# Performance work log

Measured on AMD Instinct MI355X. Metric: run time of the kernel, lower is better.

Reference implementation:

```python
import jax, jax.numpy as jnp
import numpy as np

B, IN, OUT = 8192, 4096, 4096
EPS = 1e-4


def setup_inputs() -> dict:
    key = jax.random.key(0)
    k1, k2 = jax.random.split(key)
    x = jax.random.normal(k1, (B, IN), dtype=jnp.float32)
    gamma = jnp.ones((IN,), dtype=jnp.float32)
    beta = jnp.zeros((IN,), dtype=jnp.float32)
    weight = jax.random.normal(k2, (OUT, IN), dtype=jnp.float32) * 0.02
    bias = jnp.zeros((OUT,), dtype=jnp.float32)
    return {"x": x, "gamma": gamma, "beta": beta, "weight": weight, "bias": bias}


def bin_weight(w):
    # center per output row, clamp, L1-scale, sign (2D branch of BinWeightFn)
    wc = jnp.clip(w - jnp.mean(w, axis=1, keepdims=True), -1.0, 1.0)
    n = w.shape[1]
    scale = jnp.sum(jnp.abs(wc), axis=1, keepdims=True) / n  # [out, 1]
    return jnp.sign(wc), scale


def reference(x, gamma, beta, weight, bias):
    # BatchNorm1d in training mode: batch statistics (biased variance)
    mu = jnp.mean(x, axis=0)
    var = jnp.var(x, axis=0)
    xn = (x - mu) / jnp.sqrt(var + EPS) * gamma + beta
    # binarize activations and weights
    x_bin = jnp.sign(xn)
    w_bin, scale = bin_weight(weight)
    # binary GEMM + bias, then per-output-channel L1 scale, then ReLU
    y = x_bin @ w_bin.T + bias          # [B, OUT]
    y = y * scale.reshape(1, -1)
    return jax.nn.relu(y)
```

## Files before the change

kernel.cpp:

```cpp
#include <hip/hip_runtime.h>
#include <stdint.h>

#define BATCH 8192
#define IN 4096
#define OUT 4096
#define EPS 1e-4f
#define RCHUNK 128
#define NCHUNKS (BATCH / RCHUNK)

typedef int v4i __attribute__((ext_vector_type(4)));

#define AS1(p) ((const __attribute__((address_space(1))) void*)(p))
#define AS3(p) ((__attribute__((address_space(3))) void*)(p))

__global__ __launch_bounds__(256) void colstat_partial(
    const float* __restrict__ x, float* __restrict__ P1, float* __restrict__ P2) {
    int col = blockIdx.x * 256 + threadIdx.x;
    int r0 = blockIdx.y * RCHUNK;
    float s1 = 0.f, s2 = 0.f;
    const float* p = x + (size_t)r0 * IN + col;
    for (int r = 0; r < RCHUNK; ++r) {
        float v = p[(size_t)r * IN];
        s1 += v;
        s2 += v * v;
    }
    P1[blockIdx.y * IN + col] = s1;
    P2[blockIdx.y * IN + col] = s2;
}

__global__ __launch_bounds__(256) void colstat_final(
    const float* __restrict__ P1, const float* __restrict__ P2,
    const float* __restrict__ gamma, float* __restrict__ mu, float* __restrict__ aArr) {
    int col = blockIdx.x * 256 + threadIdx.x;
    double s1 = 0.0, s2 = 0.0;
    for (int c = 0; c < NCHUNKS; ++c) {
        s1 += (double)P1[c * IN + col];
        s2 += (double)P2[c * IN + col];
    }
    double m = s1 / (double)BATCH;
    double var = s2 / (double)BATCH - m * m;
    float rstd = (float)(1.0 / sqrt(var + (double)EPS));
    mu[col] = (float)m;
    aArr[col] = rstd * gamma[col];
}

__global__ __launch_bounds__(256) void binx8(
    const float* __restrict__ x, const float* __restrict__ mu,
    const float* __restrict__ aArr, const float* __restrict__ beta,
    uint8_t* __restrict__ x01, int* __restrict__ px) {
    __shared__ int red[4];
    int r = blockIdx.x;
    int tid = threadIdx.x;
    int lane = tid & 63;
    int wv = tid >> 6;
    const float4* row = (const float4*)(x + (size_t)r * IN);
    const float4* m4 = (const float4*)mu;
    const float4* a4 = (const float4*)aArr;
    const float4* b4 = (const float4*)beta;
    uchar4* o4 = (uchar4*)(x01 + (size_t)r * IN);
    int cnt = 0;
#pragma unroll
    for (int it = 0; it < IN / 1024; ++it) {
        int q = it * 256 + tid;
        float4 v = row[q];
        float4 m = m4[q];
        float4 a = a4[q];
        float4 b = b4[q];
        uchar4 ob;
        ob.x = (uint8_t)((v.x - m.x) * a.x + b.x > 0.f);
        ob.y = (uint8_t)((v.y - m.y) * a.y + b.y > 0.f);
        ob.z = (uint8_t)((v.z - m.z) * a.z + b.z > 0.f);
        ob.w = (uint8_t)((v.w - m.w) * a.w + b.w > 0.f);
        cnt += (int)ob.x + (int)ob.y + (int)ob.z + (int)ob.w;
        o4[q] = ob;
    }
    for (int off = 32; off > 0; off >>= 1) cnt += __shfl_down(cnt, off, 64);
    if (lane == 0) red[wv] = cnt;
    __syncthreads();
    if (tid == 0) px[r] = red[0] + red[1] + red[2] + red[3];
}

__global__ __launch_bounds__(256) void binw8(
    const float* __restrict__ w, uint8_t* __restrict__ w01,
    float* __restrict__ scale, int* __restrict__ pw) {
    __shared__ double redd[4];
    __shared__ int redi[4];
    __shared__ double bcast;
    int o = blockIdx.x;
    int tid = threadIdx.x;
    int lane = tid & 63;
    int wv = tid >> 6;
    const float4* row = (const float4*)(w + (size_t)o * IN);
    uchar4* o4 = (uchar4*)(w01 + (size_t)o * IN);

    float4 vs[4];
    float part = 0.f;
#pragma unroll
    for (int it = 0; it < 4; ++it) {
        vs[it] = row[it * 256 + tid];
        part += vs[it].x + vs[it].y + vs[it].z + vs[it].w;
    }
    double d = (double)part;
    for (int off = 32; off > 0; off >>= 1) d += __shfl_down(d, off, 64);
    if (lane == 0) redd[wv] = d;
    __syncthreads();
    if (tid == 0) bcast = (redd[0] + redd[1] + redd[2] + redd[3]) / (double)IN;
    __syncthreads();
    float mean = (float)bcast;

    float absacc = 0.f;
    int cnt = 0;
#pragma unroll
    for (int it = 0; it < 4; ++it) {
        float4 v = vs[it];
        float wcx = v.x - mean, wcy = v.y - mean, wcz = v.z - mean, wcw = v.w - mean;
        uchar4 ob;
        ob.x = (uint8_t)(wcx > 0.f);
        ob.y = (uint8_t)(wcy > 0.f);
        ob.z = (uint8_t)(wcz > 0.f);
        ob.w = (uint8_t)(wcw > 0.f);
        cnt += (int)ob.x + (int)ob.y + (int)ob.z + (int)ob.w;
        absacc += fminf(fabsf(wcx), 1.0f) + fminf(fabsf(wcy), 1.0f) +
                  fminf(fabsf(wcz), 1.0f) + fminf(fabsf(wcw), 1.0f);
        o4[it * 256 + tid] = ob;
    }
    double da = (double)absacc;
    for (int off = 32; off > 0; off >>= 1) da += __shfl_down(da, off, 64);
    for (int off = 32; off > 0; off >>= 1) cnt += __shfl_down(cnt, off, 64);
    if (lane == 0) { redd[wv] = da; redi[wv] = cnt; }
    __syncthreads();
    if (tid == 0) {
        scale[o] = (float)((redd[0] + redd[1] + redd[2] + redd[3]) / (double)IN);
        pw[o] = redi[0] + redi[1] + redi[2] + redi[3];
    }
}

#define BM 128
#define BN 128
#define BKI 64
__global__ __launch_bounds__(256, 2) void bgemm_i8(
    const uint8_t* __restrict__ x01, const uint8_t* __restrict__ w01,
    const int* __restrict__ px, const int* __restrict__ pw,
    const float* __restrict__ scale, const float* __restrict__ bias,
    float* __restrict__ out) {
    __shared__ uint8_t As[BM * BKI];
    __shared__ uint8_t Bs[BN * BKI];

    int tid = threadIdx.x;
    int lane = tid & 63;
    int wave = tid >> 6;
    int rowBlk = blockIdx.y * BM;
    int colBlk = blockIdx.x * BN;
    int wm = (wave >> 1) * 64;
    int wn = (wave & 1) * 64;

    v4i acc[4][4];
#pragma unroll
    for (int i = 0; i < 4; ++i)
#pragma unroll
        for (int j = 0; j < 4; ++j) acc[i][j] = (v4i){0, 0, 0, 0};

    const uint8_t* ag = x01 + (size_t)rowBlk * IN;
    const uint8_t* bg = w01 + (size_t)colBlk * IN;

    int lrow = lane & 15;
    int lk = (lane >> 4) * 16;

    for (int kc = 0; kc < IN / BKI; ++kc) {
#pragma unroll
        for (int it = 0; it < 2; ++it) {
            int idx = tid + it * 256;
            int r = idx >> 2;
            int ch = idx & 3;
            __builtin_amdgcn_global_load_lds(
                AS1(ag + (size_t)r * IN + kc * BKI + ch * 16),
                AS3(As + idx * 16), 16, 0, 0);
            __builtin_amdgcn_global_load_lds(
                AS1(bg + (size_t)r * IN + kc * BKI + ch * 16),
                AS3(Bs + idx * 16), 16, 0, 0);
        }
        __syncthreads();

        v4i af[4], bf[4];
#pragma unroll
        for (int i = 0; i < 4; ++i)
            af[i] = *(const v4i*)(As + (wm + i * 16 + lrow) * BKI + lk);
#pragma unroll
        for (int j = 0; j < 4; ++j)
            bf[j] = *(const v4i*)(Bs + (wn + j * 16 + lrow) * BKI + lk);
#pragma unroll
        for (int i = 0; i < 4; ++i)
#pragma unroll
            for (int j = 0; j < 4; ++j)
                acc[i][j] = __builtin_amdgcn_mfma_i32_16x16x64_i8(af[i], bf[j], acc[i][j], 0, 0, 0);
        __syncthreads();
    }

    int crow0 = (lane >> 4) * 4;
    int ccol = lane & 15;
#pragma unroll
    for (int i = 0; i < 4; ++i) {
        int rbase = rowBlk + wm + i * 16 + crow0;
        int pxr[4];
#pragma unroll
        for (int rg = 0; rg < 4; ++rg) pxr[rg] = px[rbase + rg];
#pragma unroll
        for (int j = 0; j < 4; ++j) {
            int cb = colBlk + wn + j * 16 + ccol;
            float sc = scale[cb];
            float bs = bias[cb];
            int pwc = pw[cb];
#pragma unroll
            for (int rg = 0; rg < 4; ++rg) {
                int dot = 4 * acc[i][j][rg] - 2 * pxr[rg] - 2 * pwc + IN;
                float y = ((float)dot + bs) * sc;
                out[(size_t)(rbase + rg) * OUT + cb] = y > 0.f ? y : 0.f;
            }
        }
    }
}

extern "C" void kernel_launch(void* const* d_in, const int* in_sizes, int n_in,
                              void* d_out, int out_size, void* d_ws, size_t ws_size,
                              hipStream_t stream) {
    const float* x = (const float*)d_in[0];
    const float* gamma = (const float*)d_in[1];
    const float* beta = (const float*)d_in[2];
    const float* weight = (const float*)d_in[3];
    const float* bias = (const float*)d_in[4];
    float* out = (float*)d_out;

    char* w = (char*)d_ws;
    float* mu = (float*)(w);
    float* aArr = (float*)(w + 16384);
    float* scale = (float*)(w + 32768);
    int* px = (int*)(w + 49152);
    int* pw = (int*)(w + 81920);
    float* P1 = (float*)(w + (1 << 20));
    float* P2 = (float*)(w + (2 << 20));
    uint8_t* x01 = (uint8_t*)(w + (4 << 20));
    uint8_t* w01 = (uint8_t*)(w + (36 << 20));

    colstat_partial<<<dim3(IN / 256, NCHUNKS), 256, 0, stream>>>(x, P1, P2);
    colstat_final<<<dim3(IN / 256), 256, 0, stream>>>(P1, P2, gamma, mu, aArr);
    binx8<<<dim3(BATCH), 256, 0, stream>>>(x, mu, aArr, beta, x01, px);
    binw8<<<dim3(OUT), 256, 0, stream>>>(weight, w01, scale, pw);
    bgemm_i8<<<dim3(OUT / BN, BATCH / BM), 256, 0, stream>>>(x01, w01, px, pw, scale, bias, out);
}
```

Baseline: 450.3 us.

## Rewrite int8 binary GEMM as 256x256 tile ping-pong pipelined kernel

Replaces the 128x128 single-buffered int8 MFMA GEMM with a 512-thread 256x256 tile kernel. It uses double-buffered 128KB LDS with XOR-swizzled layout, interleaved async global-to-LDS staging, manual barriers and vmcnt waits, setprio around MFMA bursts, and a swizzled block order for L2 reuse. It also vectorizes the column-stat partial kernel to float4. The aim is to hide load latency, cut LDS bank conflicts and raise arithmetic intensity. The cost is heavy register use, one block per CU of LDS, and fragile hand-tuned wait counts.

After: 412.2 us. 8.4% less time.

```diff
diff --git a/kernel.cpp b/kernel.cpp
--- a/kernel.cpp
+++ b/kernel.cpp
@@ -9,23 +9,24 @@
 #define NCHUNKS (BATCH / RCHUNK)
 
 typedef int v4i __attribute__((ext_vector_type(4)));
+typedef unsigned char u8;
 
 #define AS1(p) ((const __attribute__((address_space(1))) void*)(p))
 #define AS3(p) ((__attribute__((address_space(3))) void*)(p))
 
 __global__ __launch_bounds__(256) void colstat_partial(
     const float* __restrict__ x, float* __restrict__ P1, float* __restrict__ P2) {
-    int col = blockIdx.x * 256 + threadIdx.x;
+    int c4 = blockIdx.x * 256 + threadIdx.x;
     int r0 = blockIdx.y * RCHUNK;
-    float s1 = 0.f, s2 = 0.f;
-    const float* p = x + (size_t)r0 * IN + col;
+    float4 s1 = {0.f, 0.f, 0.f, 0.f}, s2 = {0.f, 0.f, 0.f, 0.f};
+    const float4* p = (const float4*)x + (size_t)r0 * (IN / 4) + c4;
     for (int r = 0; r < RCHUNK; ++r) {
-        float v = p[(size_t)r * IN];
-        s1 += v;
-        s2 += v * v;
-    }
-    P1[blockIdx.y * IN + col] = s1;
-    P2[blockIdx.y * IN + col] = s2;
+        float4 v = p[(size_t)r * (IN / 4)];
+        s1.x += v.x; s1.y += v.y; s1.z += v.z; s1.w += v.w;
+        s2.x += v.x * v.x; s2.y += v.y * v.y; s2.z += v.z * v.z; s2.w += v.w * v.w;
+    }
+    ((float4*)P1)[blockIdx.y * (IN / 4) + c4] = s1;
+    ((float4*)P2)[blockIdx.y * (IN / 4) + c4] = s2;
 }
 
 __global__ __launch_bounds__(256) void colstat_final(
@@ -47,7 +48,7 @@
 __global__ __launch_bounds__(256) void binx8(
     const float* __restrict__ x, const float* __restrict__ mu,
     const float* __restrict__ aArr, const float* __restrict__ beta,
-    uint8_t* __restrict__ x01, int* __restrict__ px) {
+    u8* __restrict__ x01, int* __restrict__ px) {
     __shared__ int red[4];
     int r = blockIdx.x;
     int tid = threadIdx.x;
@@ -67,10 +68,10 @@
         float4 a = a4[q];
         float4 b = b4[q];
         uchar4 ob;
-        ob.x = (uint8_t)((v.x - m.x) * a.x + b.x > 0.f);
-        ob.y = (uint8_t)((v.y - m.y) * a.y + b.y > 0.f);
-        ob.z = (uint8_t)((v.z - m.z) * a.z + b.z > 0.f);
-        ob.w = (uint8_t)((v.w - m.w) * a.w + b.w > 0.f);
+        ob.x = (u8)((v.x - m.x) * a.x + b.x > 0.f);
+        ob.y = (u8)((v.y - m.y) * a.y + b.y > 0.f);
+        ob.z = (u8)((v.z - m.z) * a.z + b.z > 0.f);
+        ob.w = (u8)((v.w - m.w) * a.w + b.w > 0.f);
         cnt += (int)ob.x + (int)ob.y + (int)ob.z + (int)ob.w;
         o4[q] = ob;
     }
@@ -81,7 +82,7 @@
 }
 
 __global__ __launch_bounds__(256) void binw8(
-    const float* __restrict__ w, uint8_t* __restrict__ w01,
+    const float* __restrict__ w, u8* __restrict__ w01,
     float* __restrict__ scale, int* __restrict__ pw) {
     __shared__ double redd[4];
     __shared__ int redi[4];
@@ -115,10 +116,10 @@
         float4 v = vs[it];
         float wcx = v.x - mean, wcy = v.y - mean, wcz = v.z - mean, wcw = v.w - mean;
         uchar4 ob;
-        ob.x = (uint8_t)(wcx > 0.f);
-        ob.y = (uint8_t)(wcy > 0.f);
-        ob.z = (uint8_t)(wcz > 0.f);
-        ob.w = (uint8_t)(wcw > 0.f);
+        ob.x = (u8)(wcx > 0.f);
+        ob.y = (u8)(wcy > 0.f);
+        ob.z = (u8)(wcz > 0.f);
+        ob.w = (u8)(wcw > 0.f);
         cnt += (int)ob.x + (int)ob.y + (int)ob.z + (int)ob.w;
         absacc += fminf(fabsf(wcx), 1.0f) + fminf(fabsf(wcy), 1.0f) +
                   fminf(fabsf(wcz), 1.0f) + fminf(fabsf(wcw), 1.0f);
@@ -135,78 +136,146 @@
     }
 }
 
-#define BM 128
-#define BN 128
-#define BKI 64
-__global__ __launch_bounds__(256, 2) void bgemm_i8(
-    const uint8_t* __restrict__ x01, const uint8_t* __restrict__ w01,
+#define BKB 128
+#define NKT (IN / BKB)
+#define NIT (NKT / 2)
+
+#define STG_A(t, q, p) __builtin_amdgcn_global_load_lds( \
+    AS1(ag + (size_t)((q)*64 + slr) * IN + (t)*BKB + sswz), \
+    AS3(lds + (p)*65536 + (q)*8192 + sdst), 16, 0, 0)
+#define STG_B(t, q, p) __builtin_amdgcn_global_load_lds( \
+    AS1(bg + (size_t)((q)*64 + slr) * IN + (t)*BKB + sswz), \
+    AS3(lds + (p)*65536 + 32768 + (q)*8192 + sdst), 16, 0, 0)
+
+#define LOADA(p, rh) do { \
+    _Pragma("unroll") for (int i_ = 0; i_ < 4; ++i_) \
+    _Pragma("unroll") for (int k_ = 0; k_ < 2; ++k_) \
+        af[i_][k_] = *(const v4i*)(lds + (p)*65536 + aBase + (rh)*8192 + i_*2048 + swk[k_]); \
+} while (0)
+#define LOADB(p, ch) do { \
+    _Pragma("unroll") for (int j_ = 0; j_ < 2; ++j_) \
+    _Pragma("unroll") for (int k_ = 0; k_ < 2; ++k_) \
+        bf[j_][k_] = *(const v4i*)(lds + (p)*65536 + bBase + (ch)*4096 + j_*2048 + swk[k_]); \
+} while (0)
+#define MMA(rh, ch) do { \
+    __builtin_amdgcn_s_setprio(1); \
+    _Pragma("unroll") for (int i_ = 0; i_ < 4; ++i_) \
+    _Pragma("unroll") for (int j_ = 0; j_ < 2; ++j_) \
+    _Pragma("unroll") for (int k_ = 0; k_ < 2; ++k_) \
+        acc[(rh)*4 + i_][(ch)*2 + j_] = __builtin_amdgcn_mfma_i32_16x16x64_i8( \
+            af[i_][k_], bf[j_][k_], acc[(rh)*4 + i_][(ch)*2 + j_], 0, 0, 0); \
+    __builtin_amdgcn_s_setprio(0); \
+} while (0)
+#define BAR() asm volatile("s_barrier" ::: "memory")
+#define VM(n) asm volatile("s_waitcnt vmcnt(" #n ")" ::: "memory")
+
+__global__ __launch_bounds__(512, 2) void bgemm_i8(
+    const u8* __restrict__ x01, const u8* __restrict__ w01,
     const int* __restrict__ px, const int* __restrict__ pw,
     const float* __restrict__ scale, const float* __restrict__ bias,
     float* __restrict__ out) {
-    __shared__ uint8_t As[BM * BKI];
-    __shared__ uint8_t Bs[BN * BKI];
+    __shared__ u8 lds[131072];
 
     int tid = threadIdx.x;
     int lane = tid & 63;
     int wave = tid >> 6;
-    int rowBlk = blockIdx.y * BM;
-    int colBlk = blockIdx.x * BN;
-    int wm = (wave >> 1) * 64;
-    int wn = (wave & 1) * 64;
-
-    v4i acc[4][4];
-#pragma unroll
-    for (int i = 0; i < 4; ++i)
+    int wm = wave >> 2;
+    int wn = wave & 3;
+
+    int lin = blockIdx.y * (OUT / 256) + blockIdx.x;
+    int swz = (lin & 7) * 64 + (lin >> 3);
+    int colBlk = (swz & 15) * 256;
+    int rowBlk = (swz >> 4) * 256;
+
+    const u8* ag = x01 + (size_t)rowBlk * IN;
+    const u8* bg = w01 + (size_t)colBlk * IN;
+
+    int slr = tid >> 3;
+    int ss = tid & 7;
+    int sswz = (ss ^ (slr & 7)) * 16;
+    int sdst = slr * 128 + ss * 16;
+
+    int lrow = lane & 15;
+    int lhi = lane >> 4;
+    int llo = lane & 7;
+    int swk[2] = { ((lhi) ^ llo) * 16, ((4 + lhi) ^ llo) * 16 };
+    int aBase = (wm * 128 + lrow) * 128;
+    int bBase = 32768 + (wn * 64 + lrow) * 128;
+
+    v4i acc[8][4];
+#pragma unroll
+    for (int i = 0; i < 8; ++i)
 #pragma unroll
         for (int j = 0; j < 4; ++j) acc[i][j] = (v4i){0, 0, 0, 0};
-
-    const uint8_t* ag = x01 + (size_t)rowBlk * IN;
-    const uint8_t* bg = w01 + (size_t)colBlk * IN;
-
-    int lrow = lane & 15;
-    int lk = (lane >> 4) * 16;
-
-    for (int kc = 0; kc < IN / BKI; ++kc) {
-#pragma unroll
-        for (int it = 0; it < 2; ++it) {
-            int idx = tid + it * 256;
-            int r = idx >> 2;
-            int ch = idx & 3;
-            __builtin_amdgcn_global_load_lds(
-                AS1(ag + (size_t)r * IN + kc * BKI + ch * 16),
-                AS3(As + idx * 16), 16, 0, 0);
-            __builtin_amdgcn_global_load_lds(
-                AS1(bg + (size_t)r * IN + kc * BKI + ch * 16),
-                AS3(Bs + idx * 16), 16, 0, 0);
-        }
-        __syncthreads();
-
-        v4i af[4], bf[4];
-#pragma unroll
-        for (int i = 0; i < 4; ++i)
-            af[i] = *(const v4i*)(As + (wm + i * 16 + lrow) * BKI + lk);
-#pragma unroll
-        for (int j = 0; j < 4; ++j)
-            bf[j] = *(const v4i*)(Bs + (wn + j * 16 + lrow) * BKI + lk);
-#pragma unroll
-        for (int i = 0; i < 4; ++i)
-#pragma unroll
-            for (int j = 0; j < 4; ++j)
-                acc[i][j] = __builtin_amdgcn_mfma_i32_16x16x64_i8(af[i], bf[j], acc[i][j], 0, 0, 0);
-        __syncthreads();
-    }
-
-    int crow0 = (lane >> 4) * 4;
-    int ccol = lane & 15;
-#pragma unroll
-    for (int i = 0; i < 4; ++i) {
-        int rbase = rowBlk + wm + i * 16 + crow0;
+    v4i af[4][2], bf[2][2];
+
+    STG_A(0, 0, 0); STG_A(0, 1, 0); STG_A(0, 2, 0); STG_A(0, 3, 0);
+    STG_B(0, 0, 0); STG_B(0, 1, 0); STG_B(0, 2, 0); STG_B(0, 3, 0);
+    STG_A(1, 0, 1); STG_A(1, 2, 1);
+    VM(2);
+    BAR();
+
+    for (int j = 0; j < NIT - 1; ++j) {
+        int O = 2 * j + 1, E2 = 2 * j + 2, O2 = 2 * j + 3;
+        LOADA(0, 0); LOADB(0, 0);
+        STG_B(O, 0, 1); STG_B(O, 1, 1);
+        BAR(); MMA(0, 0); BAR();
+        LOADB(0, 1);
+        STG_B(O, 2, 1); STG_B(O, 3, 1);
+        BAR(); MMA(0, 1); VM(6); BAR();
+        LOADA(0, 1); LOADB(0, 0);
+        STG_A(O, 1, 1); STG_A(O, 3, 1); STG_A(E2, 0, 0); STG_A(E2, 2, 0);
+        BAR(); MMA(1, 0); BAR();
+        LOADB(0, 1);
+        BAR(); MMA(1, 1); VM(4); BAR();
+        LOADA(1, 0); LOADB(1, 0);
+        STG_B(E2, 0, 0); STG_B(E2, 1, 0);
+        BAR(); MMA(0, 0); BAR();
+        LOADB(1, 1);
+        STG_B(E2, 2, 0); STG_B(E2, 3, 0);
+        BAR(); MMA(0, 1); VM(4); BAR();
+        LOADA(1, 1); LOADB(1, 0);
+        STG_A(E2, 1, 0); STG_A(E2, 3, 0);
+        BAR(); MMA(1, 0); BAR();
+        LOADB(1, 1);
+        STG_A(O2, 0, 1); STG_A(O2, 2, 1);
+        BAR(); MMA(1, 1); VM(4); BAR();
+    }
+
+    {
+        int O = NKT - 1;
+        LOADA(0, 0); LOADB(0, 0);
+        STG_B(O, 0, 1); STG_B(O, 1, 1);
+        BAR(); MMA(0, 0); BAR();
+        LOADB(0, 1);
+        STG_B(O, 2, 1); STG_B(O, 3, 1);
+        BAR(); MMA(0, 1); VM(6); BAR();
+        LOADA(0, 1); LOADB(0, 0);
+        STG_A(O, 1, 1); STG_A(O, 3, 1);
+        BAR(); MMA(1, 0); BAR();
+        LOADB(0, 1);
+        BAR(); MMA(1, 1); VM(2); BAR();
+        LOADA(1, 0); LOADB(1, 0);
+        BAR(); MMA(0, 0); BAR();
+        LOADB(1, 1);
+        BAR(); MMA(0, 1); VM(0); BAR();
+        LOADA(1, 1); LOADB(1, 0);
+        BAR(); MMA(1, 0); BAR();
+        LOADB(1, 1);
+        BAR(); MMA(1, 1); BAR();
+    }
+
+    int crow0 = lhi * 4;
+    int ccol = lrow;
+#pragma unroll
+    for (int i = 0; i < 8; ++i) {
+        int rbase = rowBlk + wm * 128 + i * 16 + crow0;
         int pxr[4];
 #pragma unroll
         for (int rg = 0; rg < 4; ++rg) pxr[rg] = px[rbase + rg];
 #pragma unroll
         for (int j = 0; j < 4; ++j) {
-            int cb = colBlk + wn + j * 16 + ccol;
+            int cb = colBlk + wn * 64 + j * 16 + ccol;
             float sc = scale[cb];
             float bs = bias[cb];
             int pwc = pw[cb];
@@ -238,12 +307,12 @@
     int* pw = (int*)(w + 81920);
     float* P1 = (float*)(w + (1 << 20));
     float* P2 = (float*)(w + (2 << 20));
-    uint8_t* x01 = (uint8_t*)(w + (4 << 20));
-    uint8_t* w01 = (uint8_t*)(w + (36 << 20));
-
-    colstat_partial<<<dim3(IN / 256, NCHUNKS), 256, 0, stream>>>(x, P1, P2);
+    u8* x01 = (u8*)(w + (4 << 20));
+    u8* w01 = (u8*)(w + (36 << 20));
+
+    colstat_partial<<<dim3(IN / 1024, NCHUNKS), 256, 0, stream>>>(x, P1, P2);
     colstat_final<<<dim3(IN / 256), 256, 0, stream>>>(P1, P2, gamma, mu, aArr);
     binx8<<<dim3(BATCH), 256, 0, stream>>>(x, mu, aArr, beta, x01, px);
     binw8<<<dim3(OUT), 256, 0, stream>>>(weight, w01, scale, pw);
-    bgemm_i8<<<dim3(OUT / BN, BATCH / BM), 256, 0, stream>>>(x01, w01, px, pw, scale, bias, out);
-}
+    bgemm_i8<<<dim3(OUT / 256, BATCH / 256), 512, 0, stream>>>(x01, w01, px, pw, scale, bias, out);
+}
```
